# Performance work log

Hardware: AMD Instinct MI355X
Metric: run time of the kernel (lower is better)

Reference implementation:

```python
import jax, jax.numpy as jnp
import numpy as np


def setup_inputs() -> dict:
    key = jax.random.key(0)
    k1, k2 = jax.random.split(key)
    B, N, C, H, W = 16, 10000, 3, 32, 32
    x = jax.random.normal(k1, (B, C, H, W), dtype=jnp.float32)
    images = jax.random.normal(k2, (N, C, H, W), dtype=jnp.float32)
    # sval = schedule(t) in (0,1); bt^2 = sval, at = sqrt(1 - sval)
    sval = jnp.asarray(0.5, dtype=jnp.float32)
    return {"x": x, "images": images, "sval": sval}


def reference(x, images, sval):
    # Original math: pwise = x[:,None] - at*images[None]
    #   weights = softmax(-||pwise||^2 / (2 bt^2), over N)
    #   out = -sum_n weights_n * pwise_n / bt^2
    # We decompose ||x - at*img||^2 = ||x||^2 - 2 at x.img + at^2 ||img||^2
    # (GEMM form) and use sum_n w_n (x - at*img_n) = x - at*(w @ imgs),
    # avoiding the [B,N,C,H,W] intermediate. Identical math.
    bt2 = sval                      # bt^2 = schedule(t)
    at = jnp.sqrt(1.0 - sval)       # at = sqrt(1 - schedule(t))
    B = x.shape[0]
    N = images.shape[0]
    xf = x.reshape(B, -1)           # [B, D]
    imf = images.reshape(N, -1)     # [N, D]
    x_sq = jnp.sum(xf * xf, axis=-1)        # [B]
    i_sq = jnp.sum(imf * imf, axis=-1)      # [N]
    cross = xf @ imf.T                      # [B, N]  (main GEMM)
    weight_args = -(x_sq[:, None] - 2.0 * at * cross
                    + (at * at) * i_sq[None, :]) / (2.0 * bt2)
    weights = jax.nn.softmax(weight_args, axis=1)   # [B, N]
    mix = weights @ imf                             # [B, D]
    out = -(xf - at * mix) / bt2                    # [B, D]
    return out.reshape(x.shape)
```

## Files before the change

### kernel.cpp

```cpp
#include <hip/hip_runtime.h>
#include <math.h>

#define BB 16
#define NN 10000
#define DD 3072
#define SEL_CUT 40.0f
#define CAP 1024

typedef const float __attribute__((address_space(1)))* gas_t;
typedef float __attribute__((address_space(3)))* las_t;

#define RSTEP2(arr, mm, cc)                                             \
  {                                                                     \
    const bool up = (lane & (mm)) != 0;                                 \
    _Pragma("unroll")                                                   \
    for (int k = 0; k < (cc); ++k) {                                    \
      float2 lo = arr[k], hi = arr[k + (cc)];                           \
      float sx = up ? lo.x : hi.x, sy = up ? lo.y : hi.y;               \
      float rx = __shfl_xor(sx, (mm), 64);                              \
      float ry = __shfl_xor(sy, (mm), 64);                              \
      arr[k].x = (up ? hi.x : lo.x) + rx;                               \
      arr[k].y = (up ? hi.y : lo.y) + ry;                               \
    }                                                                   \
  }
#define RFULL(arr)                                                      \
  RSTEP2(arr, 32, 8)                                                    \
  RSTEP2(arr, 16, 4)                                                    \
  RSTEP2(arr, 8, 2)                                                     \
  RSTEP2(arr, 4, 1)                                                     \
  arr[0].x += __shfl_xor(arr[0].x, 2, 64);                              \
  arr[0].y += __shfl_xor(arr[0].y, 2, 64);                              \
  arr[0].x += __shfl_xor(arr[0].x, 1, 64);                              \
  arr[0].y += __shfl_xor(arr[0].y, 1, 64);

__global__ __launch_bounds__(256) void k1_args(
    const float* __restrict__ x, const float* __restrict__ images,
    const float* __restrict__ svalp, float* __restrict__ args)
{
  __shared__ float xs[2][BB * 256];
  const int t = threadIdx.x;
  const int lane = t & 63;
  const int wave = t >> 6;
  const int n0 = (blockIdx.x * 4 + wave) * 4;
  const int dl = lane << 2;

  const float* __restrict__ r0 = images + (size_t)(n0 + 0) * DD;
  const float* __restrict__ r1 = images + (size_t)(n0 + 1) * DD;
  const float* __restrict__ r2 = images + (size_t)(n0 + 2) * DD;
  const float* __restrict__ r3 = images + (size_t)(n0 + 3) * DD;

  float2 acc0[BB], acc1[BB];
  float2 isq0 = make_float2(0.f, 0.f), isq1 = make_float2(0.f, 0.f);
#pragma unroll
  for (int b = 0; b < BB; ++b) {
    acc0[b] = make_float2(0.f, 0.f);
    acc1[b] = make_float2(0.f, 0.f);
  }

#pragma unroll
  for (int i = 0; i < 4; ++i) {
    const int b = wave * 4 + i;
    __builtin_amdgcn_global_load_lds((gas_t)(x + b * DD + dl),
                                     (las_t)(&xs[0][b * 256]), 16, 0, 0);
  }

  float4 c0 = *(const float4*)&r0[dl];
  float4 c1 = *(const float4*)&r1[dl];
  float4 c2 = *(const float4*)&r2[dl];
  float4 c3 = *(const float4*)&r3[dl];

#pragma unroll 1
  for (int c = 0; c < 12; ++c) {
    __syncthreads();

    if (c < 11) {
      const int dn = (c + 1) * 256;
#pragma unroll
      for (int i = 0; i < 4; ++i) {
        const int b = wave * 4 + i;
        __builtin_amdgcn_global_load_lds((gas_t)(x + b * DD + dn + dl),
                                         (las_t)(&xs[(c + 1) & 1][b * 256]),
                                         16, 0, 0);
      }
    }

    float4 A0 = c0, A1 = c1, A2 = c2, A3 = c3;
    if (c < 11) {
      const int dn = (c + 1) * 256 + dl;
      c0 = *(const float4*)&r0[dn];
      c1 = *(const float4*)&r1[dn];
      c2 = *(const float4*)&r2[dn];
      c3 = *(const float4*)&r3[dn];
    }

    isq0.x += A0.x * A0.x + A0.y * A0.y + A0.z * A0.z + A0.w * A0.w;
    isq0.y += A1.x * A1.x + A1.y * A1.y + A1.z * A1.z + A1.w * A1.w;
    isq1.x += A2.x * A2.x + A2.y * A2.y + A2.z * A2.z + A2.w * A2.w;
    isq1.y += A3.x * A3.x + A3.y * A3.y + A3.z * A3.z + A3.w * A3.w;

    const float* xb = &xs[c & 1][dl];
#pragma unroll
    for (int b = 0; b < BB; ++b) {
      float4 xv = *(const float4*)&xb[b * 256];
      acc0[b].x += A0.x * xv.x + A0.y * xv.y + A0.z * xv.z + A0.w * xv.w;
      acc0[b].y += A1.x * xv.x + A1.y * xv.y + A1.z * xv.z + A1.w * xv.w;
      acc1[b].x += A2.x * xv.x + A2.y * xv.y + A2.z * xv.z + A2.w * xv.w;
      acc1[b].y += A3.x * xv.x + A3.y * xv.y + A3.z * xv.z + A3.w * xv.w;
    }
  }

  RFULL(acc0)
  RFULL(acc1)
#pragma unroll
  for (int m = 32; m >= 1; m >>= 1) {
    isq0.x += __shfl_xor(isq0.x, m, 64);
    isq0.y += __shfl_xor(isq0.y, m, 64);
    isq1.x += __shfl_xor(isq1.x, m, 64);
    isq1.y += __shfl_xor(isq1.y, m, 64);
  }

  const float sval = *svalp;
  const float at = sqrtf(1.f - sval);
  const float k1c = at / sval;
  const float k2c = (1.f - sval) / (2.f * sval);

  const int r = lane & 1;
  const int bb = (lane >> 2) & 15;
  if ((lane & 2) == 0) {
    float d0 = r ? acc0[0].y : acc0[0].x;
    float s0 = r ? isq0.y    : isq0.x;
    args[bb * NN + (n0 + r)] = k1c * d0 - k2c * s0;
    float d1 = r ? acc1[0].y : acc1[0].x;
    float s1 = r ? isq1.y    : isq1.x;
    args[bb * NN + (n0 + 2 + r)] = k1c * d1 - k2c * s1;
  }
}

__global__ __launch_bounds__(1024) void k2_select(
    const float* __restrict__ args, int* __restrict__ cnt,
    int* __restrict__ idx, float* __restrict__ wv)
{
  __shared__ float red[16];
  __shared__ float mshared, lshared;
  const int b = blockIdx.x;
  const int t = threadIdx.x;
  const int lane = t & 63, wave = t >> 6;
  if (t == 0) cnt[b] = 0;

  float a[10];
#pragma unroll
  for (int i = 0; i < 10; ++i) {
    int n = t + (i << 10);
    a[i] = (n < NN) ? args[b * NN + n] : -INFINITY;
  }

  float mx = -INFINITY;
#pragma unroll
  for (int i = 0; i < 10; ++i) mx = fmaxf(mx, a[i]);
#pragma unroll
  for (int m = 32; m >= 1; m >>= 1) mx = fmaxf(mx, __shfl_xor(mx, m, 64));
  if (lane == 0) red[wave] = mx;
  __syncthreads();
  if (wave == 0) {
    float v = (lane < 16) ? red[lane] : -INFINITY;
#pragma unroll
    for (int m = 8; m >= 1; m >>= 1) v = fmaxf(v, __shfl_xor(v, m, 64));
    if (lane == 0) mshared = v;
  }
  __syncthreads();
  mx = mshared;

  float s = 0.f;
#pragma unroll
  for (int i = 0; i < 10; ++i) s += __expf(a[i] - mx);
#pragma unroll
  for (int m = 32; m >= 1; m >>= 1) s += __shfl_xor(s, m, 64);
  if (lane == 0) red[wave] = s;
  __syncthreads();
  if (wave == 0) {
    float v = (lane < 16) ? red[lane] : 0.f;
#pragma unroll
    for (int m = 8; m >= 1; m >>= 1) v += __shfl_xor(v, m, 64);
    if (lane == 0) lshared = v;
  }
  __syncthreads();
  const float invl = 1.f / lshared;

#pragma unroll
  for (int i = 0; i < 10; ++i) {
    if (a[i] > mx - SEL_CUT) {
      int k = atomicAdd(&cnt[b], 1);
      if (k < CAP) {
        idx[b * CAP + k] = t + (i << 10);
        wv[b * CAP + k] = __expf(a[i] - mx) * invl;
      }
    }
  }
}

__global__ __launch_bounds__(256) void k3_sparse(
    const float* __restrict__ images, const float* __restrict__ x,
    const float* __restrict__ svalp, const int* __restrict__ cnt,
    const int* __restrict__ idx, const float* __restrict__ wv,
    float* __restrict__ out)
{
  const int b = blockIdx.y;
  const int d0 = blockIdx.x * 1024 + (threadIdx.x << 2);
  int c = cnt[b];
  if (c > CAP) c = CAP;

  float4 acc = make_float4(0.f, 0.f, 0.f, 0.f);
  for (int j = 0; j < c; ++j) {
    int n = idx[b * CAP + j];
    float w = wv[b * CAP + j];
    float4 im = *(const float4*)&images[(size_t)n * DD + d0];
    acc.x += w * im.x; acc.y += w * im.y;
    acc.z += w * im.z; acc.w += w * im.w;
  }

  const float sval = *svalp;
  const float at = sqrtf(1.f - sval);
  const float inv_bt2 = 1.f / sval;
  float4 xv = *(const float4*)&x[b * DD + d0];
  float4 o;
  o.x = (at * acc.x - xv.x) * inv_bt2;
  o.y = (at * acc.y - xv.y) * inv_bt2;
  o.z = (at * acc.z - xv.z) * inv_bt2;
  o.w = (at * acc.w - xv.w) * inv_bt2;
  *(float4*)&out[b * DD + d0] = o;
}

extern "C" void kernel_launch(void* const* d_in, const int* in_sizes, int n_in,
                              void* d_out, int out_size, void* d_ws, size_t ws_size,
                              hipStream_t stream) {
  const float* x      = (const float*)d_in[0];
  const float* images = (const float*)d_in[1];
  const float* sval   = (const float*)d_in[2];
  float* out = (float*)d_out;
  float* ws  = (float*)d_ws;

  float* args = ws;
  int*   cnt  = (int*)(ws + 160000);
  int*   idx  = (int*)(ws + 160032);
  float* wv   = ws + 176416;

  hipLaunchKernelGGL(k1_args, dim3(625), dim3(256), 0, stream,
                     x, images, sval, args);
  hipLaunchKernelGGL(k2_select, dim3(16), dim3(1024), 0, stream,
                     args, cnt, idx, wv);
  hipLaunchKernelGGL(k3_sparse, dim3(3, 16), dim3(256), 0, stream,
                     images, x, sval, cnt, idx, wv, out);
}
```

Baseline: 198.3 us.

## Split the args GEMM over four D-quarters and sum the partials in select

The distance/argument kernel now launches a 625x4 grid, with each block handling one quarter of the feature dimension. Each block loads its whole x quarter into LDS once, which replaces the double-buffered per-chunk reload and the per-iteration barriers. Partial arguments go to a 4x larger workspace, and the select kernel adds the four partials before the softmax. The aim is more blocks to fill the CUs and shorter serial loops per block. The costs are extra partial-result traffic and about 48KB of LDS per block, which may limit how many blocks fit on a CU at once.

```diff
diff --git a/kernel.cpp b/kernel.cpp
--- a/kernel.cpp
+++ b/kernel.cpp
@@ -4,6 +4,7 @@
 #define BB 16
 #define NN 10000
 #define DD 3072
+#define DQ 768
 #define SEL_CUT 40.0f
 #define CAP 1024
 
@@ -33,59 +34,54 @@
   arr[0].x += __shfl_xor(arr[0].x, 1, 64);                              \
   arr[0].y += __shfl_xor(arr[0].y, 1, 64);
 
-__global__ __launch_bounds__(256) void k1_args(
+__global__ __launch_bounds__(256) void k1_partial(
     const float* __restrict__ x, const float* __restrict__ images,
-    const float* __restrict__ svalp, float* __restrict__ args)
+    const float* __restrict__ svalp, float* __restrict__ pd)
 {
-  __shared__ float xs[2][BB * 256];
+  __shared__ float xs[BB * DQ];
   const int t = threadIdx.x;
   const int lane = t & 63;
   const int wave = t >> 6;
+  const int q = blockIdx.y;
+  const int qb = q * DQ;
   const int n0 = (blockIdx.x * 4 + wave) * 4;
   const int dl = lane << 2;
 
-  const float* __restrict__ r0 = images + (size_t)(n0 + 0) * DD;
-  const float* __restrict__ r1 = images + (size_t)(n0 + 1) * DD;
-  const float* __restrict__ r2 = images + (size_t)(n0 + 2) * DD;
-  const float* __restrict__ r3 = images + (size_t)(n0 + 3) * DD;
-
-  float2 acc0[BB], acc1[BB];
-  float2 isq0 = make_float2(0.f, 0.f), isq1 = make_float2(0.f, 0.f);
-#pragma unroll
-  for (int b = 0; b < BB; ++b) {
-    acc0[b] = make_float2(0.f, 0.f);
-    acc1[b] = make_float2(0.f, 0.f);
-  }
-
 #pragma unroll
   for (int i = 0; i < 4; ++i) {
     const int b = wave * 4 + i;
-    __builtin_amdgcn_global_load_lds((gas_t)(x + b * DD + dl),
-                                     (las_t)(&xs[0][b * 256]), 16, 0, 0);
-  }
+#pragma unroll
+    for (int cc = 0; cc < 3; ++cc) {
+      __builtin_amdgcn_global_load_lds(
+          (gas_t)(x + b * DD + qb + cc * 256 + dl),
+          (las_t)(&xs[b * DQ + cc * 256]), 16, 0, 0);
+    }
+  }
+
+  const float* __restrict__ r0 = images + (size_t)(n0 + 0) * DD + qb;
+  const float* __restrict__ r1 = images + (size_t)(n0 + 1) * DD + qb;
+  const float* __restrict__ r2 = images + (size_t)(n0 + 2) * DD + qb;
+  const float* __restrict__ r3 = images + (size_t)(n0 + 3) * DD + qb;
 
   float4 c0 = *(const float4*)&r0[dl];
   float4 c1 = *(const float4*)&r1[dl];
   float4 c2 = *(const float4*)&r2[dl];
   float4 c3 = *(const float4*)&r3[dl];
 
+  float2 acc0[BB], acc1[BB];
+  float2 isq0 = make_float2(0.f, 0.f), isq1 = make_float2(0.f, 0.f);
+#pragma unroll
+  for (int b = 0; b < BB; ++b) {
+    acc0[b] = make_float2(0.f, 0.f);
+    acc1[b] = make_float2(0.f, 0.f);
+  }
+
+  __syncthreads();
+
 #pragma unroll 1
-  for (int c = 0; c < 12; ++c) {
-    __syncthreads();
-
-    if (c < 11) {
-      const int dn = (c + 1) * 256;
-#pragma unroll
-      for (int i = 0; i < 4; ++i) {
-        const int b = wave * 4 + i;
-        __builtin_amdgcn_global_load_lds((gas_t)(x + b * DD + dn + dl),
-                                         (las_t)(&xs[(c + 1) & 1][b * 256]),
-                                         16, 0, 0);
-      }
-    }
-
+  for (int c = 0; c < 3; ++c) {
     float4 A0 = c0, A1 = c1, A2 = c2, A3 = c3;
-    if (c < 11) {
+    if (c < 2) {
       const int dn = (c + 1) * 256 + dl;
       c0 = *(const float4*)&r0[dn];
       c1 = *(const float4*)&r1[dn];
@@ -98,10 +94,10 @@
     isq1.x += A2.x * A2.x + A2.y * A2.y + A2.z * A2.z + A2.w * A2.w;
     isq1.y += A3.x * A3.x + A3.y * A3.y + A3.z * A3.z + A3.w * A3.w;
 
-    const float* xb = &xs[c & 1][dl];
+    const float* xb = &xs[c * 256 + dl];
 #pragma unroll
     for (int b = 0; b < BB; ++b) {
-      float4 xv = *(const float4*)&xb[b * 256];
+      float4 xv = *(const float4*)&xb[b * DQ];
       acc0[b].x += A0.x * xv.x + A0.y * xv.y + A0.z * xv.z + A0.w * xv.w;
       acc0[b].y += A1.x * xv.x + A1.y * xv.y + A1.z * xv.z + A1.w * xv.w;
       acc1[b].x += A2.x * xv.x + A2.y * xv.y + A2.z * xv.z + A2.w * xv.w;
@@ -129,15 +125,15 @@
   if ((lane & 2) == 0) {
     float d0 = r ? acc0[0].y : acc0[0].x;
     float s0 = r ? isq0.y    : isq0.x;
-    args[bb * NN + (n0 + r)] = k1c * d0 - k2c * s0;
+    pd[((size_t)q * BB + bb) * NN + (n0 + r)] = k1c * d0 - k2c * s0;
     float d1 = r ? acc1[0].y : acc1[0].x;
     float s1 = r ? isq1.y    : isq1.x;
-    args[bb * NN + (n0 + 2 + r)] = k1c * d1 - k2c * s1;
+    pd[((size_t)q * BB + bb) * NN + (n0 + 2 + r)] = k1c * d1 - k2c * s1;
   }
 }
 
 __global__ __launch_bounds__(1024) void k2_select(
-    const float* __restrict__ args, int* __restrict__ cnt,
+    const float* __restrict__ pd, int* __restrict__ cnt,
     int* __restrict__ idx, float* __restrict__ wv)
 {
   __shared__ float red[16];
@@ -151,7 +147,14 @@
 #pragma unroll
   for (int i = 0; i < 10; ++i) {
     int n = t + (i << 10);
-    a[i] = (n < NN) ? args[b * NN + n] : -INFINITY;
+    if (n < NN) {
+      a[i] = (pd[((size_t)0 * BB + b) * NN + n] +
+              pd[((size_t)1 * BB + b) * NN + n]) +
+             (pd[((size_t)2 * BB + b) * NN + n] +
+              pd[((size_t)3 * BB + b) * NN + n]);
+    } else {
+      a[i] = -INFINITY;
+    }
   }
 
   float mx = -INFINITY;
@@ -239,15 +242,15 @@
   float* out = (float*)d_out;
   float* ws  = (float*)d_ws;
 
-  float* args = ws;
-  int*   cnt  = (int*)(ws + 160000);
-  int*   idx  = (int*)(ws + 160032);
-  float* wv   = ws + 176416;
-
-  hipLaunchKernelGGL(k1_args, dim3(625), dim3(256), 0, stream,
-                     x, images, sval, args);
+  float* pd  = ws;
+  int*   cnt = (int*)(ws + 640000);
+  int*   idx = (int*)(ws + 640032);
+  float* wv  = ws + 656416;
+
+  hipLaunchKernelGGL(k1_partial, dim3(625, 4), dim3(256), 0, stream,
+                     x, images, sval, pd);
   hipLaunchKernelGGL(k2_select, dim3(16), dim3(1024), 0, stream,
-                     args, cnt, idx, wv);
+                     pd, cnt, idx, wv);
   hipLaunchKernelGGL(k3_sparse, dim3(3, 16), dim3(256), 0, stream,
                      images, x, sval, cnt, idx, wv, out);
 }
```

Result: no change. 197.6 us (-0.4%).
